# Kernel optimization log

Hardware: AMD Instinct MI355X
Metric: run time of the kernel (lower is better)

The kernel has to match this reference:

```python
import jax, jax.numpy as jnp
import numpy as np

# Tree / encoder dims (see shape_source): root + 4 middle + 16 leaves
T_DATA = 100000
T_V = 100
WIN = 2 * T_V - 1          # (T_V-1)*2 + 1 = 199, first MLP in_dim
HID = 256                  # hid_dim
N_MID = 4                  # numel(in_idx_list[0])  (middle-level latents)
N_LEAF = 16                # numel(out_idx_list[-1]) (leaf-level latents)


def setup_inputs() -> dict:
    key = jax.random.key(0)
    ks = jax.random.split(key, 6)
    sc = lambda k, shape, fan: jax.random.normal(k, shape, jnp.float32) * (1.0 / np.sqrt(fan))
    return {
        "V_in": jax.random.normal(ks[0], (T_DATA,), jnp.float32),
        "W1": sc(ks[1], (WIN, HID), WIN),
        "b1": jnp.zeros((HID,), jnp.float32),
        "W2": sc(ks[2], (HID, N_MID), HID),
        "b2": jnp.zeros((N_MID,), jnp.float32),
        # leaf_encoder = MLP(HID, HID, N_LEAF)
        "Wl1": sc(ks[3], (HID, HID), HID),
        "bl1": jnp.zeros((HID,), jnp.float32),
        "Wl2": sc(ks[4], (HID, N_LEAF), HID),
        "bl2": jnp.zeros((N_LEAF,), jnp.float32),
    }


def reference(V_in, W1, b1, W2, b2, Wl1, bl1, Wl2, bl2):
    """Vectorized LVAE_shGLM.Encoder: the original loops over every timestep t,
    slicing pad_V_in[t:t+2*T_V-1] and running MLP.encode chains per step.
    Here all T windows are processed as one batched GEMM chain.
    MLP.encode(x) = (h = relu(x@W1+b1), mu = h@W2+b2)."""
    T = V_in.shape[0]
    pad = jnp.zeros((T + 2 * (T_V - 1),), V_in.dtype).at[T_V - 1:T_V - 1 + T].set(V_in)
    idx = jnp.arange(T)[:, None] + jnp.arange(WIN)[None, :]
    windows = pad[idx]
    # middle encoder (level 0 of the dendritic tree)
    h_mid = jax.nn.relu(windows @ W1 + b1)          # [T, HID]
    mu_mid = h_mid @ W2 + b2                        # [T, N_MID]
    # leaf encoder consumes the middle hidden state
    h_leaf = jax.nn.relu(h_mid @ Wl1 + bl1)         # [T, HID]
    mu_leaf = h_leaf @ Wl2 + bl2                    # [T, N_LEAF]
    # up_mu_array[t] = [middle mus (count 0..N_MID), leaf mus (N_MID..sub_no-1)]
    return jnp.concatenate([mu_mid, mu_leaf], axis=1)  # [T, sub_no-1] = [T, 20]
```

## Files before the change

kernel.cpp:

```cpp
#include <hip/hip_runtime.h>


typedef __bf16 bf16;
typedef __bf16 bf16x8 __attribute__((ext_vector_type(8)));
typedef float  f32x4  __attribute__((ext_vector_type(4)));
typedef float  f32x16 __attribute__((ext_vector_type(16)));

constexpr int T_DATA = 100000;
constexpr int T_V    = 100;
constexpr int WIN    = 199;
constexpr int HID    = 256;
constexpr int BT     = 128;
constexpr int HSTR   = 264;
constexpr int VLEN   = 352;
constexpr int VSTR   = 360;

constexpr int PWL1_OFF = 104 * 512;
constexpr int PW2_OFF  = 232 * 512;
constexpr int PWL2_OFF = 240 * 512;

__global__ void pack_weights(const float* __restrict__ W1, const float* __restrict__ W2,
                             const float* __restrict__ Wl1, const float* __restrict__ Wl2,
                             bf16* __restrict__ ws) {
  const int gid  = blockIdx.x * blockDim.x + threadIdx.x;
  const int lane = gid & 63;
  const int grp  = gid >> 6;
  bf16x8 v;
  if (grp < 104) {
    const int kt = grp >> 3, nt = grp & 7, n = nt * 32 + (lane & 31);
#pragma unroll
    for (int j = 0; j < 8; ++j) {
      const int k = kt * 16 + (lane >> 5) * 8 + j;
      v[j] = (k < WIN) ? (bf16)W1[k * HID + n] : (bf16)0.0f;
    }
  } else if (grp < 232) {
    const int q = grp - 104;
    const int kt = q >> 3, nt = q & 7, n = nt * 32 + (lane & 31);
#pragma unroll
    for (int j = 0; j < 8; ++j) {
      const int k = kt * 16 + (lane >> 5) * 8 + j;
      v[j] = (bf16)Wl1[k * HID + n];
    }
  } else if (grp < 240) {
    const int kt = grp - 232, m = lane & 15;
#pragma unroll
    for (int j = 0; j < 8; ++j) {
      const int k = kt * 32 + (lane >> 4) * 8 + j;
      v[j] = (m < 4) ? (bf16)W2[k * 4 + m] : (bf16)0.0f;
    }
  } else {
    const int kt = grp - 240, m = lane & 15;
#pragma unroll
    for (int j = 0; j < 8; ++j) {
      const int k = kt * 32 + (lane >> 4) * 8 + j;
      v[j] = (bf16)Wl2[k * 16 + m];
    }
  }
  *reinterpret_cast<bf16x8*>(ws + (size_t)gid * 8) = v;
}

__global__ __launch_bounds__(512, 4) void fused_enc(
    const float* __restrict__ V, const float* __restrict__ b1,
    const float* __restrict__ b2, const float* __restrict__ bl1,
    const float* __restrict__ bl2, const bf16* __restrict__ ws,
    float* __restrict__ out) {
  __shared__ bf16 Vdup[8][VSTR];
  __shared__ bf16 hbuf[BT * HSTR];

  const int tid  = threadIdx.x;
  const int lane = tid & 63;
  const int w    = tid >> 6;
  const int c5   = lane & 31;
  const int hi   = lane >> 5;
  const int m    = lane & 15;
  const int g    = lane >> 4;
  const long t0  = (long)blockIdx.x * BT;

  for (int c = tid; c < 8 * VLEN; c += 512) {
    const int p = c / VLEN, q = c - p * VLEN;
    const long src = t0 + q + p - (T_V - 1);
    const float v = (src >= 0 && src < T_DATA) ? V[src] : 0.0f;
    Vdup[p][q] = (bf16)v;
  }
  __syncthreads();

  const int p  = lane & 7;
  const int qb = (c5 + hi * 8) - p;
  const bf16* vrow = &Vdup[p][0];

  f32x16 acc[4];
#pragma unroll
  for (int rt = 0; rt < 4; ++rt) acc[rt] = (f32x16){};

#pragma unroll
  for (int kt = 0; kt < 13; ++kt) {
    const bf16x8 b = *reinterpret_cast<const bf16x8*>(
        ws + (size_t)(kt * 8 + w) * 512 + lane * 8);
#pragma unroll
    for (int rt = 0; rt < 4; ++rt) {
      const bf16x8 a = *reinterpret_cast<const bf16x8*>(vrow + qb + kt * 16 + rt * 32);
      acc[rt] = __builtin_amdgcn_mfma_f32_32x32x16_bf16(a, b, acc[rt], 0, 0, 0);
    }
  }

  const int   col = w * 32 + c5;
  const float bb1 = b1[col];
#pragma unroll
  for (int rt = 0; rt < 4; ++rt)
#pragma unroll
    for (int r = 0; r < 16; ++r) {
      const int row = rt * 32 + (r & 3) + 8 * (r >> 2) + 4 * hi;
      hbuf[row * HSTR + col] = (bf16)fmaxf(acc[rt][r] + bb1, 0.0f);
    }
  __syncthreads();

#pragma unroll
  for (int rt = 0; rt < 4; ++rt) acc[rt] = (f32x16){};
#pragma unroll
  for (int kt = 0; kt < 16; ++kt) {
    const bf16x8 b = *reinterpret_cast<const bf16x8*>(
        ws + PWL1_OFF + (size_t)(kt * 8 + w) * 512 + lane * 8);
    const int koff = kt * 16 + hi * 8;
#pragma unroll
    for (int rt = 0; rt < 4; ++rt) {
      const bf16x8 a = *reinterpret_cast<const bf16x8*>(&hbuf[(rt * 32 + c5) * HSTR + koff]);
      acc[rt] = __builtin_amdgcn_mfma_f32_32x32x16_bf16(a, b, acc[rt], 0, 0, 0);
    }
  }

  f32x4 mu = {0.f, 0.f, 0.f, 0.f};
#pragma unroll
  for (int kt = 0; kt < 8; ++kt) {
    const bf16x8 a = *reinterpret_cast<const bf16x8*>(
        &hbuf[(w * 16 + m) * HSTR + kt * 32 + g * 8]);
    const bf16x8 b = *reinterpret_cast<const bf16x8*>(
        ws + PW2_OFF + (size_t)kt * 512 + lane * 8);
    mu = __builtin_amdgcn_mfma_f32_16x16x32_bf16(a, b, mu, 0, 0, 0);
  }
  {
    const float b2v = (m < 4) ? b2[m] : 0.0f;
#pragma unroll
    for (int j = 0; j < 4; ++j) {
      const long t = t0 + w * 16 + g * 4 + j;
      if (t < T_DATA && m < 4) out[t * 20 + m] = mu[j] + b2v;
    }
  }
  __syncthreads();

  const float bbl = bl1[col];
#pragma unroll
  for (int rt = 0; rt < 4; ++rt)
#pragma unroll
    for (int r = 0; r < 16; ++r) {
      const int row = rt * 32 + (r & 3) + 8 * (r >> 2) + 4 * hi;
      hbuf[row * HSTR + col] = (bf16)fmaxf(acc[rt][r] + bbl, 0.0f);
    }
  __syncthreads();

  mu = (f32x4){0.f, 0.f, 0.f, 0.f};
#pragma unroll
  for (int kq = 0; kq < 8; ++kq) {
    const bf16x8 a = *reinterpret_cast<const bf16x8*>(
        &hbuf[(w * 16 + m) * HSTR + kq * 32 + g * 8]);
    const bf16x8 b = *reinterpret_cast<const bf16x8*>(
        ws + PWL2_OFF + (size_t)kq * 512 + lane * 8);
    mu = __builtin_amdgcn_mfma_f32_16x16x32_bf16(a, b, mu, 0, 0, 0);
  }
  {
    const float blv = bl2[m];
#pragma unroll
    for (int j = 0; j < 4; ++j) {
      const long t = t0 + w * 16 + g * 4 + j;
      if (t < T_DATA) out[t * 20 + 4 + m] = mu[j] + blv;
    }
  }
}

extern "C" void kernel_launch(void* const* d_in, const int* in_sizes, int n_in,
                              void* d_out, int out_size, void* d_ws, size_t ws_size,
                              hipStream_t stream) {
  const float* V   = (const float*)d_in[0];
  const float* W1  = (const float*)d_in[1];
  const float* b1  = (const float*)d_in[2];
  const float* W2  = (const float*)d_in[3];
  const float* b2  = (const float*)d_in[4];
  const float* Wl1 = (const float*)d_in[5];
  const float* bl1 = (const float*)d_in[6];
  const float* Wl2 = (const float*)d_in[7];
  const float* bl2 = (const float*)d_in[8];
  bf16* ws = (bf16*)d_ws;
  float* out = (float*)d_out;

  pack_weights<<<62, 256, 0, stream>>>(W1, W2, Wl1, Wl2, ws);

  const int grid = (T_DATA + BT - 1) / BT;
  fused_enc<<<grid, 512, 0, stream>>>(V, b1, b2, bl1, bl2, ws, out);
}
```

Measured before the change: 42.75 us.

## Use 4 waves per block with 2x4 register tiles per wave

The block shrinks from 8 waves to 4. Each wave now computes a 64-row by 128-column tile (2 row tiles by 4 column tiles of 32x32 MFMA), so each A fragment is reused across 4 B fragments and each B across 2 A fragments. The aim is fewer LDS and global weight loads per MFMA. In exchange each wave holds 128 accumulator registers, which raises register pressure and may lower occupancy, and fewer waves share each block's LDS.

```diff
diff --git a/kernel.cpp b/kernel.cpp
--- a/kernel.cpp
+++ b/kernel.cpp
@@ -59,7 +59,7 @@
   *reinterpret_cast<bf16x8*>(ws + (size_t)gid * 8) = v;
 }
 
-__global__ __launch_bounds__(512, 4) void fused_enc(
+__global__ __launch_bounds__(256, 2) void fused_enc(
     const float* __restrict__ V, const float* __restrict__ b1,
     const float* __restrict__ b2, const float* __restrict__ bl1,
     const float* __restrict__ bl2, const bf16* __restrict__ ws,
@@ -70,13 +70,15 @@
   const int tid  = threadIdx.x;
   const int lane = tid & 63;
   const int w    = tid >> 6;
+  const int wr   = w >> 1;
+  const int wc   = w & 1;
   const int c5   = lane & 31;
   const int hi   = lane >> 5;
   const int m    = lane & 15;
   const int g    = lane >> 4;
   const long t0  = (long)blockIdx.x * BT;
 
-  for (int c = tid; c < 8 * VLEN; c += 512) {
+  for (int c = tid; c < 8 * VLEN; c += 256) {
     const int p = c / VLEN, q = c - p * VLEN;
     const long src = t0 + q + p - (T_V - 1);
     const float v = (src >= 0 && src < T_DATA) ? V[src] : 0.0f;
@@ -85,94 +87,126 @@
   __syncthreads();
 
   const int p  = lane & 7;
-  const int qb = (c5 + hi * 8) - p;
+  const int qb = (c5 + hi * 8) - p + wr * 64;
   const bf16* vrow = &Vdup[p][0];
 
-  f32x16 acc[4];
-#pragma unroll
-  for (int rt = 0; rt < 4; ++rt) acc[rt] = (f32x16){};
+  f32x16 acc[2][4];
+#pragma unroll
+  for (int rt = 0; rt < 2; ++rt)
+#pragma unroll
+    for (int c = 0; c < 4; ++c) acc[rt][c] = (f32x16){};
 
 #pragma unroll
   for (int kt = 0; kt < 13; ++kt) {
-    const bf16x8 b = *reinterpret_cast<const bf16x8*>(
-        ws + (size_t)(kt * 8 + w) * 512 + lane * 8);
-#pragma unroll
-    for (int rt = 0; rt < 4; ++rt) {
-      const bf16x8 a = *reinterpret_cast<const bf16x8*>(vrow + qb + kt * 16 + rt * 32);
-      acc[rt] = __builtin_amdgcn_mfma_f32_32x32x16_bf16(a, b, acc[rt], 0, 0, 0);
-    }
-  }
-
-  const int   col = w * 32 + c5;
-  const float bb1 = b1[col];
-#pragma unroll
-  for (int rt = 0; rt < 4; ++rt)
-#pragma unroll
-    for (int r = 0; r < 16; ++r) {
-      const int row = rt * 32 + (r & 3) + 8 * (r >> 2) + 4 * hi;
-      hbuf[row * HSTR + col] = (bf16)fmaxf(acc[rt][r] + bb1, 0.0f);
-    }
-  __syncthreads();
-
-#pragma unroll
-  for (int rt = 0; rt < 4; ++rt) acc[rt] = (f32x16){};
+    bf16x8 bfr[4];
+#pragma unroll
+    for (int c = 0; c < 4; ++c)
+      bfr[c] = *reinterpret_cast<const bf16x8*>(
+          ws + (size_t)(kt * 8 + wc * 4 + c) * 512 + lane * 8);
+#pragma unroll
+    for (int rt = 0; rt < 2; ++rt) {
+      const bf16x8 a = *reinterpret_cast<const bf16x8*>(vrow + qb + rt * 32 + kt * 16);
+#pragma unroll
+      for (int c = 0; c < 4; ++c)
+        acc[rt][c] = __builtin_amdgcn_mfma_f32_32x32x16_bf16(a, bfr[c], acc[rt][c], 0, 0, 0);
+    }
+  }
+
+#pragma unroll
+  for (int c = 0; c < 4; ++c) {
+    const int col = wc * 128 + c * 32 + c5;
+    const float bb = b1[col];
+#pragma unroll
+    for (int rt = 0; rt < 2; ++rt)
+#pragma unroll
+      for (int r = 0; r < 16; ++r) {
+        const int row = wr * 64 + rt * 32 + (r & 3) + 8 * (r >> 2) + 4 * hi;
+        hbuf[row * HSTR + col] = (bf16)fmaxf(acc[rt][c][r] + bb, 0.0f);
+      }
+  }
+  __syncthreads();
+
+#pragma unroll
+  for (int rt = 0; rt < 2; ++rt)
+#pragma unroll
+    for (int c = 0; c < 4; ++c) acc[rt][c] = (f32x16){};
 #pragma unroll
   for (int kt = 0; kt < 16; ++kt) {
-    const bf16x8 b = *reinterpret_cast<const bf16x8*>(
-        ws + PWL1_OFF + (size_t)(kt * 8 + w) * 512 + lane * 8);
+    bf16x8 bfr[4];
+#pragma unroll
+    for (int c = 0; c < 4; ++c)
+      bfr[c] = *reinterpret_cast<const bf16x8*>(
+          ws + PWL1_OFF + (size_t)(kt * 8 + wc * 4 + c) * 512 + lane * 8);
     const int koff = kt * 16 + hi * 8;
 #pragma unroll
-    for (int rt = 0; rt < 4; ++rt) {
-      const bf16x8 a = *reinterpret_cast<const bf16x8*>(&hbuf[(rt * 32 + c5) * HSTR + koff]);
-      acc[rt] = __builtin_amdgcn_mfma_f32_32x32x16_bf16(a, b, acc[rt], 0, 0, 0);
-    }
-  }
-
-  f32x4 mu = {0.f, 0.f, 0.f, 0.f};
+    for (int rt = 0; rt < 2; ++rt) {
+      const bf16x8 a = *reinterpret_cast<const bf16x8*>(
+          &hbuf[(wr * 64 + rt * 32 + c5) * HSTR + koff]);
+#pragma unroll
+      for (int c = 0; c < 4; ++c)
+        acc[rt][c] = __builtin_amdgcn_mfma_f32_32x32x16_bf16(a, bfr[c], acc[rt][c], 0, 0, 0);
+    }
+  }
+
+  f32x4 mu2a[2] = {(f32x4){0.f, 0.f, 0.f, 0.f}, (f32x4){0.f, 0.f, 0.f, 0.f}};
 #pragma unroll
   for (int kt = 0; kt < 8; ++kt) {
-    const bf16x8 a = *reinterpret_cast<const bf16x8*>(
-        &hbuf[(w * 16 + m) * HSTR + kt * 32 + g * 8]);
-    const bf16x8 b = *reinterpret_cast<const bf16x8*>(
+    const bf16x8 bw2 = *reinterpret_cast<const bf16x8*>(
         ws + PW2_OFF + (size_t)kt * 512 + lane * 8);
-    mu = __builtin_amdgcn_mfma_f32_16x16x32_bf16(a, b, mu, 0, 0, 0);
+#pragma unroll
+    for (int q = 0; q < 2; ++q) {
+      const bf16x8 a = *reinterpret_cast<const bf16x8*>(
+          &hbuf[(w * 32 + q * 16 + m) * HSTR + kt * 32 + g * 8]);
+      mu2a[q] = __builtin_amdgcn_mfma_f32_16x16x32_bf16(a, bw2, mu2a[q], 0, 0, 0);
+    }
   }
   {
     const float b2v = (m < 4) ? b2[m] : 0.0f;
 #pragma unroll
-    for (int j = 0; j < 4; ++j) {
-      const long t = t0 + w * 16 + g * 4 + j;
-      if (t < T_DATA && m < 4) out[t * 20 + m] = mu[j] + b2v;
-    }
-  }
-  __syncthreads();
-
-  const float bbl = bl1[col];
-#pragma unroll
-  for (int rt = 0; rt < 4; ++rt)
-#pragma unroll
-    for (int r = 0; r < 16; ++r) {
-      const int row = rt * 32 + (r & 3) + 8 * (r >> 2) + 4 * hi;
-      hbuf[row * HSTR + col] = (bf16)fmaxf(acc[rt][r] + bbl, 0.0f);
-    }
-  __syncthreads();
-
-  mu = (f32x4){0.f, 0.f, 0.f, 0.f};
+    for (int q = 0; q < 2; ++q)
+#pragma unroll
+      for (int j = 0; j < 4; ++j) {
+        const long t = t0 + w * 32 + q * 16 + g * 4 + j;
+        if (t < T_DATA && m < 4) out[t * 20 + m] = mu2a[q][j] + b2v;
+      }
+  }
+  __syncthreads();
+
+#pragma unroll
+  for (int c = 0; c < 4; ++c) {
+    const int col = wc * 128 + c * 32 + c5;
+    const float bb = bl1[col];
+#pragma unroll
+    for (int rt = 0; rt < 2; ++rt)
+#pragma unroll
+      for (int r = 0; r < 16; ++r) {
+        const int row = wr * 64 + rt * 32 + (r & 3) + 8 * (r >> 2) + 4 * hi;
+        hbuf[row * HSTR + col] = (bf16)fmaxf(acc[rt][c][r] + bb, 0.0f);
+      }
+  }
+  __syncthreads();
+
+  f32x4 mu4a[2] = {(f32x4){0.f, 0.f, 0.f, 0.f}, (f32x4){0.f, 0.f, 0.f, 0.f}};
 #pragma unroll
   for (int kq = 0; kq < 8; ++kq) {
-    const bf16x8 a = *reinterpret_cast<const bf16x8*>(
-        &hbuf[(w * 16 + m) * HSTR + kq * 32 + g * 8]);
     const bf16x8 b = *reinterpret_cast<const bf16x8*>(
         ws + PWL2_OFF + (size_t)kq * 512 + lane * 8);
-    mu = __builtin_amdgcn_mfma_f32_16x16x32_bf16(a, b, mu, 0, 0, 0);
+#pragma unroll
+    for (int q = 0; q < 2; ++q) {
+      const bf16x8 a = *reinterpret_cast<const bf16x8*>(
+          &hbuf[(w * 32 + q * 16 + m) * HSTR + kq * 32 + g * 8]);
+      mu4a[q] = __builtin_amdgcn_mfma_f32_16x16x32_bf16(a, b, mu4a[q], 0, 0, 0);
+    }
   }
   {
     const float blv = bl2[m];
 #pragma unroll
-    for (int j = 0; j < 4; ++j) {
-      const long t = t0 + w * 16 + g * 4 + j;
-      if (t < T_DATA) out[t * 20 + 4 + m] = mu[j] + blv;
-    }
+    for (int q = 0; q < 2; ++q)
+#pragma unroll
+      for (int j = 0; j < 4; ++j) {
+        const long t = t0 + w * 32 + q * 16 + g * 4 + j;
+        if (t < T_DATA) out[t * 20 + 4 + m] = mu4a[q][j] + blv;
+      }
   }
 }
 
@@ -194,5 +228,5 @@
   pack_weights<<<62, 256, 0, stream>>>(W1, W2, Wl1, Wl2, ws);
 
   const int grid = (T_DATA + BT - 1) / BT;
-  fused_enc<<<grid, 512, 0, stream>>>(V, b1, b2, bl1, bl2, ws, out);
+  fused_enc<<<grid, 256, 0, stream>>>(V, b1, b2, bl1, bl2, ws, out);
 }
```

Measured after the change: 53.04 us. 24.1% more time.
